# Kernel tuning notes

Measured on AMD Instinct MI355X. Metric: run time of the kernel, lower is better.

## Reference

```python
import jax, jax.numpy as jnp
import numpy as np

N_NODES = 50000
N_EDGES = 800000
D_S, D_R, D_E, D_X, D_P, NUM_CLASSES = 64, 16, 64, 16, 64, 10


def setup_inputs() -> dict:
    key = jax.random.key(0)
    ks = jax.random.split(key, 11)
    return {
        "O": jax.random.normal(ks[0], (N_NODES, D_S), dtype=jnp.float32),
        "X": jax.random.normal(ks[1], (N_NODES, D_X), dtype=jnp.float32),
        "R_a": jax.random.normal(ks[2], (N_EDGES, D_R), dtype=jnp.float32),
        "senders": jax.random.randint(ks[3], (N_EDGES,), 0, N_NODES, dtype=jnp.int32).astype(jnp.int64),
        "receivers": jax.random.randint(ks[4], (N_EDGES,), 0, N_NODES, dtype=jnp.int32).astype(jnp.int64),
        "W_r": jax.random.normal(ks[5], (2 * D_S + D_R, D_E), dtype=jnp.float32) * 0.05,
        "b_r": jax.random.normal(ks[6], (D_E,), dtype=jnp.float32) * 0.05,
        "W_o": jax.random.normal(ks[7], (D_S + D_X + D_E, D_P), dtype=jnp.float32) * 0.05,
        "b_o": jax.random.normal(ks[8], (D_P,), dtype=jnp.float32) * 0.05,
        "W_s": jax.random.normal(ks[9], (D_P, NUM_CLASSES), dtype=jnp.float32) * 0.05,
        "b_s": jax.random.normal(ks[10], (NUM_CLASSES,), dtype=jnp.float32) * 0.05,
    }


def reference(O, X, R_a, senders, receivers, W_r, b_r, W_o, b_o, W_s, b_s):
    n_nodes = O.shape[0]
    # marshalling: gather sender/receiver node states, concat relation attrs -> [E, 2*D_S + D_R]
    B = jnp.concatenate([O[senders], O[receivers], R_a], axis=-1)
    # relation model phi_r: per-edge effects [E, D_E]
    E = B @ W_r + b_r
    # scatter-aggregate edge effects onto receiver nodes -> [N, D_E]
    E_hat = jax.ops.segment_sum(E, receivers, num_segments=n_nodes)
    # object model phi_o on concat(state, external, aggregated effects)
    C = jnp.concatenate([O, X, E_hat], axis=-1)
    P = C @ W_o + b_o
    scores = P @ W_s + b_s
    probs = jax.nn.softmax(scores, axis=1)
    return probs
```

## Files before the change

kernel.cpp:

```cpp
#include <hip/hip_runtime.h>

#define N_NODES 50000
#define N_EDGES 800000

#define WS_A       ((size_t)0)
#define WS_COUNT   ((size_t)16384)
#define WS_CURSOR  ((size_t)216384)
#define WS_OFF     ((size_t)217088)
#define WS_RANK    ((size_t)417792)
#define WS_US      ((size_t)3618816)
#define WS_U01     ((size_t)6019072)
#define WS_WSORT   ((size_t)10019328)

__device__ __forceinline__ unsigned int f32_to_bf16_rne(float f) {
    unsigned int x = __float_as_uint(f);
    return (x + 0x7fffu + ((x >> 16) & 1u)) >> 16;
}

__global__ __launch_bounds__(256) void precompute_A(
    const float* __restrict__ W_r, const float* __restrict__ b_r,
    const float* __restrict__ W_o, const float* __restrict__ b_o,
    const float* __restrict__ W_s, const float* __restrict__ b_s,
    float* __restrict__ A)
{
    __shared__ float Wc2[640];
    const int t = threadIdx.x;

    for (int idx = t; idx < 640; idx += 256) {
        const int row = 80 + idx / 10, c = idx % 10;
        float acc = 0.f;
        for (int j = 0; j < 64; ++j)
            acc = fmaf(W_o[row * 64 + j], W_s[j * 10 + c], acc);
        Wc2[idx] = acc;
    }
    __syncthreads();

    for (int g = blockIdx.x * 256 + t; g < 3616; g += gridDim.x * 256) {
        if (g < 1356) {
            const int row = g / 6, c = 10 + g % 6;
            A[row * 16 + c] = 0.f;
        } else if (g < 2156) {
            const int i = g - 1356, row = i / 10, c = i % 10;
            float acc = 0.f;
            for (int j = 0; j < 64; ++j)
                acc = fmaf(W_o[row * 64 + j], W_s[j * 10 + c], acc);
            A[row * 16 + c] = acc;
        } else if (g < 3596) {
            const int i = g - 2156, k = i / 10, c = i % 10;
            const int wrow = (k < 64) ? k : (k < 80 ? 128 + (k - 64) : 64 + (k - 80));
            const int arow = (k < 64) ? 80 + k : (k < 80 ? 144 + (k - 64) : 160 + (k - 80));
            const float* src = W_r + (size_t)wrow * 64;
            float acc = 0.f;
            for (int m = 0; m < 64; ++m)
                acc = fmaf(src[m], Wc2[m * 10 + c], acc);
            A[arow * 16 + c] = acc;
        } else if (g < 3606) {
            const int c = g - 3596;
            float acc = 0.f;
            for (int m = 0; m < 64; ++m)
                acc = fmaf(b_r[m], Wc2[m * 10 + c], acc);
            A[224 * 16 + c] = acc;
        } else {
            const int c = g - 3606;
            float acc = b_s[c];
            for (int j = 0; j < 64; ++j)
                acc = fmaf(b_o[j], W_s[j * 10 + c], acc);
            A[225 * 16 + c] = acc;
        }
    }
}

__global__ __launch_bounds__(256) void node_u_kernel(
    const float* __restrict__ O, const float* __restrict__ X,
    const float* __restrict__ A,
    float* __restrict__ us, float* __restrict__ u01)
{
    __shared__ float2 lA[226 * 5];
    const int t = threadIdx.x;
    for (int i = t; i < 226 * 5; i += 256) {
        const int row = i / 5, cp = i - row * 5;
        lA[i] = *reinterpret_cast<const float2*>(A + (size_t)row * 16 + 2 * cp);
    }
    __syncthreads();

    const int tid = blockIdx.x * 256 + t;
    if (tid >= N_NODES * 5) return;
    const int n = tid / 5;
    const int cp = tid - n * 5;

    float vs0 = 0.f, vs1 = 0.f, v00 = 0.f, v01 = 0.f, v10 = 0.f, v11 = 0.f;

    const float4* Ov = reinterpret_cast<const float4*>(O + (size_t)n * 64);
#pragma unroll
    for (int kc = 0; kc < 16; ++kc) {
        const float4 o4 = Ov[kc];
#pragma unroll
        for (int j = 0; j < 4; ++j) {
            const float ov = (j == 0) ? o4.x : (j == 1) ? o4.y : (j == 2) ? o4.z : o4.w;
            const int k = kc * 4 + j;
            const float2 aO = lA[k * 5 + cp];
            const float2 aS = lA[(80 + k) * 5 + cp];
            const float2 aD = lA[(160 + k) * 5 + cp];
            v00 = fmaf(ov, aO.x, v00); v01 = fmaf(ov, aO.y, v01);
            vs0 = fmaf(ov, aS.x, vs0); vs1 = fmaf(ov, aS.y, vs1);
            v10 = fmaf(ov, aD.x, v10); v11 = fmaf(ov, aD.y, v11);
        }
    }
    const float4* Xv = reinterpret_cast<const float4*>(X + (size_t)n * 16);
#pragma unroll
    for (int kc = 0; kc < 4; ++kc) {
        const float4 x4 = Xv[kc];
#pragma unroll
        for (int j = 0; j < 4; ++j) {
            const float xv = (j == 0) ? x4.x : (j == 1) ? x4.y : (j == 2) ? x4.z : x4.w;
            const int k = 64 + kc * 4 + j;
            const float2 aX = lA[k * 5 + cp];
            v00 = fmaf(xv, aX.x, v00); v01 = fmaf(xv, aX.y, v01);
        }
    }

    const float2 c0 = lA[224 * 5 + cp];
    const float2 c1 = lA[225 * 5 + cp];
    *reinterpret_cast<float2*>(us + (size_t)n * 12 + 2 * cp) = make_float2(vs0, vs1);
    *reinterpret_cast<float2*>(u01 + (size_t)n * 20 + 2 * cp) =
        make_float2(v00 + c1.x, v01 + c1.y);
    *reinterpret_cast<float2*>(u01 + (size_t)n * 20 + 10 + 2 * cp) =
        make_float2(v10 + c0.x, v11 + c0.y);
}

__global__ __launch_bounds__(256) void count_rank_kernel(
    const int* __restrict__ receivers, int* __restrict__ count,
    int* __restrict__ rank)
{
    const int t = blockIdx.x * 256 + threadIdx.x;
    if (t * 4 >= N_EDGES) return;
    const int4 r4 = reinterpret_cast<const int4*>(receivers)[t];
    int4 k4;
    k4.x = atomicAdd(count + r4.x, 1);
    k4.y = atomicAdd(count + r4.y, 1);
    k4.z = atomicAdd(count + r4.z, 1);
    k4.w = atomicAdd(count + r4.w, 1);
    reinterpret_cast<int4*>(rank)[t] = k4;
}

__global__ __launch_bounds__(256) void alloc_kernel(
    const int* __restrict__ count, unsigned int* __restrict__ cursor,
    int* __restrict__ off)
{
    const int n = blockIdx.x * 256 + threadIdx.x;
    const int lane = threadIdx.x & 63;
    const int c = (n < N_NODES) ? count[n] : 0;

    int pre = c;
#pragma unroll
    for (int d = 1; d < 64; d <<= 1) {
        const int v = __shfl_up(pre, d);
        if (lane >= d) pre += v;
    }
    const int total = __shfl(pre, 63);
    int base = 0;
    if (lane == 63) base = (int)atomicAdd(cursor, (unsigned int)total);
    base = __shfl(base, 63);

    if (n < N_NODES) off[n] = base + pre - c;
}

__global__ __launch_bounds__(256) void edge_w_kernel(
    const float* __restrict__ R_a,
    const int* __restrict__ senders, const int* __restrict__ receivers,
    const int* __restrict__ rank, const int* __restrict__ off,
    const float* __restrict__ us, const float* __restrict__ A,
    unsigned int* __restrict__ wsort)
{
    const int e = blockIdx.x * blockDim.x + threadIdx.x;
    if (e >= N_EDGES) return;
    const int s = senders[e];
    const int r = receivers[e];
    const int pos = off[r] + rank[e];

    const float4* U = reinterpret_cast<const float4*>(us + (size_t)s * 12);
    const float4 ua = U[0];
    const float4 ub = U[1];
    const float4 uc = U[2];
    float a[10] = {ua.x, ua.y, ua.z, ua.w, ub.x, ub.y, ub.z, ub.w, uc.x, uc.y};

    const float4* Rv = reinterpret_cast<const float4*>(R_a + (size_t)e * 16);
#pragma unroll
    for (int kc = 0; kc < 4; ++kc) {
        const float4 b4 = Rv[kc];
        const float* A0 = A + (size_t)(144 + kc * 4) * 16;
#pragma unroll
        for (int c = 0; c < 10; ++c) a[c] = fmaf(b4.x, A0[c], a[c]);
#pragma unroll
        for (int c = 0; c < 10; ++c) a[c] = fmaf(b4.y, A0[16 + c], a[c]);
#pragma unroll
        for (int c = 0; c < 10; ++c) a[c] = fmaf(b4.z, A0[32 + c], a[c]);
#pragma unroll
        for (int c = 0; c < 10; ++c) a[c] = fmaf(b4.w, A0[48 + c], a[c]);
    }

    unsigned int* wp = wsort + (size_t)pos * 5;
    wp[0] = f32_to_bf16_rne(a[0]) | (f32_to_bf16_rne(a[1]) << 16);
    wp[1] = f32_to_bf16_rne(a[2]) | (f32_to_bf16_rne(a[3]) << 16);
    wp[2] = f32_to_bf16_rne(a[4]) | (f32_to_bf16_rne(a[5]) << 16);
    wp[3] = f32_to_bf16_rne(a[6]) | (f32_to_bf16_rne(a[7]) << 16);
    wp[4] = f32_to_bf16_rne(a[8]) | (f32_to_bf16_rne(a[9]) << 16);
}

__global__ __launch_bounds__(256) void node_score_kernel(
    const float* __restrict__ u01,
    const int* __restrict__ off, const int* __restrict__ count,
    const unsigned int* __restrict__ w,
    float* __restrict__ out)
{
    const int tid = blockIdx.x * 256 + threadIdx.x;
    const int n = tid >> 4;
    const int c = tid & 15;
    if (n >= N_NODES) return;

    const int cc = (c < 10) ? c : 0;
    const int half = cc >> 1;
    const int sh = (cc & 1) * 16;

    const int beg = off[n];
    const int dge = count[n];
    const int end = beg + dge;
    float sc = u01[(size_t)n * 20 + cc] + (float)dge * u01[(size_t)n * 20 + 10 + cc];

    float s0 = 0.f, s1 = 0.f, s2 = 0.f, s3 = 0.f;
    int i = beg;
    for (; i + 3 < end; i += 4) {
        const unsigned int v0 = w[(size_t)(i + 0) * 5 + half];
        const unsigned int v1 = w[(size_t)(i + 1) * 5 + half];
        const unsigned int v2 = w[(size_t)(i + 2) * 5 + half];
        const unsigned int v3 = w[(size_t)(i + 3) * 5 + half];
        s0 += __uint_as_float((v0 >> sh) << 16);
        s1 += __uint_as_float((v1 >> sh) << 16);
        s2 += __uint_as_float((v2 >> sh) << 16);
        s3 += __uint_as_float((v3 >> sh) << 16);
    }
    for (; i < end; ++i) {
        const unsigned int v = w[(size_t)i * 5 + half];
        s0 += __uint_as_float((v >> sh) << 16);
    }
    sc += (s0 + s1) + (s2 + s3);

    float m = (c < 10) ? sc : -3.0e38f;
#pragma unroll
    for (int d = 1; d < 16; d <<= 1) m = fmaxf(m, __shfl_xor(m, d, 16));
    const float ex = (c < 10) ? __expf(sc - m) : 0.f;
    float sum = ex;
#pragma unroll
    for (int d = 1; d < 16; d <<= 1) sum += __shfl_xor(sum, d, 16);
    if (c < 10) out[(size_t)n * 10 + c] = ex / sum;
}

extern "C" void kernel_launch(void* const* d_in, const int* in_sizes, int n_in,
                              void* d_out, int out_size, void* d_ws, size_t ws_size,
                              hipStream_t stream)
{
    const float* O    = (const float*)d_in[0];
    const float* X    = (const float*)d_in[1];
    const float* R_a  = (const float*)d_in[2];
    const int* senders   = (const int*)d_in[3];
    const int* receivers = (const int*)d_in[4];
    const float* W_r  = (const float*)d_in[5];
    const float* b_r  = (const float*)d_in[6];
    const float* W_o  = (const float*)d_in[7];
    const float* b_o  = (const float*)d_in[8];
    const float* W_s  = (const float*)d_in[9];
    const float* b_s  = (const float*)d_in[10];
    float* out = (float*)d_out;
    char* ws = (char*)d_ws;

    float* A      = (float*)(ws + WS_A);
    int* count    = (int*)(ws + WS_COUNT);
    unsigned int* cursor = (unsigned int*)(ws + WS_CURSOR);
    int* off      = (int*)(ws + WS_OFF);
    int* rank     = (int*)(ws + WS_RANK);
    float* us     = (float*)(ws + WS_US);
    float* u01    = (float*)(ws + WS_U01);
    unsigned int* wsort = (unsigned int*)(ws + WS_WSORT);

    hipMemsetAsync(count, 0, (size_t)(200000 + 4 + 384), stream);

    precompute_A<<<10, 256, 0, stream>>>(W_r, b_r, W_o, b_o, W_s, b_s, A);

    count_rank_kernel<<<(N_EDGES / 4 + 255) / 256, 256, 0, stream>>>(
        receivers, count, rank);

    alloc_kernel<<<(N_NODES + 255) / 256, 256, 0, stream>>>(count, cursor, off);

    node_u_kernel<<<(N_NODES * 5 + 255) / 256, 256, 0, stream>>>(O, X, A, us, u01);

    edge_w_kernel<<<(N_EDGES + 255) / 256, 256, 0, stream>>>(
        R_a, senders, receivers, rank, off, us, A, wsort);

    node_score_kernel<<<(N_NODES * 16 + 255) / 256, 256, 0, stream>>>(
        u01, off, count, wsort, out);
}
```

Before: 125.7 us.

## Replace per-node CSR sort with coarse 64-bin partition and LDS atomic reduction

Drops the per-receiver count/rank/offset pipeline, which needed global atomics on every edge plus a full node scan. Edges are now histogrammed into 64 bins of contiguous receivers, scattered per bin with block-local atomics, and each bin is reduced by a 1024-thread block using shared-memory float atomics before the softmax. This removes the node-level global atomics and the random CSR writes. In exchange, only 64 blocks run the final reduce, so GPU occupancy is low and LDS atomic contention rises. Float atomic accumulation order also becomes nondeterministic.

```diff
diff --git a/kernel.cpp b/kernel.cpp
--- a/kernel.cpp
+++ b/kernel.cpp
@@ -2,15 +2,18 @@
 
 #define N_NODES 50000
 #define N_EDGES 800000
+#define NBINS 64
+#define BIN_NODES 784
+#define EPB 1024
+#define NBLK_E ((N_EDGES + EPB - 1) / EPB)
 
 #define WS_A       ((size_t)0)
-#define WS_COUNT   ((size_t)16384)
-#define WS_CURSOR  ((size_t)216384)
-#define WS_OFF     ((size_t)217088)
-#define WS_RANK    ((size_t)417792)
-#define WS_US      ((size_t)3618816)
-#define WS_U01     ((size_t)6019072)
-#define WS_WSORT   ((size_t)10019328)
+#define WS_BCOUNT  ((size_t)16384)
+#define WS_BBASE   ((size_t)20480)
+#define WS_BCUR    ((size_t)20992)
+#define WS_US      ((size_t)65536)
+#define WS_U01     ((size_t)2465536)
+#define WS_PAY     ((size_t)6465536)
 
 __device__ __forceinline__ unsigned int f32_to_bf16_rne(float f) {
     unsigned int x = __float_as_uint(f);
@@ -128,131 +131,171 @@
         make_float2(v10 + c0.x, v11 + c0.y);
 }
 
-__global__ __launch_bounds__(256) void count_rank_kernel(
-    const int* __restrict__ receivers, int* __restrict__ count,
-    int* __restrict__ rank)
-{
-    const int t = blockIdx.x * 256 + threadIdx.x;
-    if (t * 4 >= N_EDGES) return;
-    const int4 r4 = reinterpret_cast<const int4*>(receivers)[t];
-    int4 k4;
-    k4.x = atomicAdd(count + r4.x, 1);
-    k4.y = atomicAdd(count + r4.y, 1);
-    k4.z = atomicAdd(count + r4.z, 1);
-    k4.w = atomicAdd(count + r4.w, 1);
-    reinterpret_cast<int4*>(rank)[t] = k4;
-}
-
-__global__ __launch_bounds__(256) void alloc_kernel(
-    const int* __restrict__ count, unsigned int* __restrict__ cursor,
-    int* __restrict__ off)
-{
-    const int n = blockIdx.x * 256 + threadIdx.x;
-    const int lane = threadIdx.x & 63;
-    const int c = (n < N_NODES) ? count[n] : 0;
-
-    int pre = c;
+__global__ __launch_bounds__(256) void hist_kernel(
+    const int* __restrict__ receivers, int* __restrict__ bcount)
+{
+    __shared__ int h[NBINS];
+    const int t = threadIdx.x;
+    if (t < NBINS) h[t] = 0;
+    __syncthreads();
+    const int t4 = blockIdx.x * 256 + t;
+    if (t4 * 4 < N_EDGES) {
+        const int4 r4 = reinterpret_cast<const int4*>(receivers)[t4];
+        atomicAdd(&h[r4.x / BIN_NODES], 1);
+        atomicAdd(&h[r4.y / BIN_NODES], 1);
+        atomicAdd(&h[r4.z / BIN_NODES], 1);
+        atomicAdd(&h[r4.w / BIN_NODES], 1);
+    }
+    __syncthreads();
+    if (t < NBINS && h[t] > 0) atomicAdd(bcount + t * 16, h[t]);
+}
+
+__global__ __launch_bounds__(64) void scan_kernel(
+    const int* __restrict__ bcount, int* __restrict__ bbase, int* __restrict__ bcur)
+{
+    const int t = threadIdx.x;
+    const int v = bcount[t * 16];
+    int pre = v;
 #pragma unroll
     for (int d = 1; d < 64; d <<= 1) {
-        const int v = __shfl_up(pre, d);
-        if (lane >= d) pre += v;
-    }
-    const int total = __shfl(pre, 63);
-    int base = 0;
-    if (lane == 63) base = (int)atomicAdd(cursor, (unsigned int)total);
-    base = __shfl(base, 63);
-
-    if (n < N_NODES) off[n] = base + pre - c;
-}
-
-__global__ __launch_bounds__(256) void edge_w_kernel(
+        const int u = __shfl_up(pre, d);
+        if (t >= d) pre += u;
+    }
+    const int ex = pre - v;
+    bbase[t] = ex;
+    bcur[t * 16] = ex;
+    if (t == 63) bbase[64] = pre;
+}
+
+__global__ __launch_bounds__(256) void bin_scatter_kernel(
     const float* __restrict__ R_a,
     const int* __restrict__ senders, const int* __restrict__ receivers,
-    const int* __restrict__ rank, const int* __restrict__ off,
     const float* __restrict__ us, const float* __restrict__ A,
-    unsigned int* __restrict__ wsort)
-{
-    const int e = blockIdx.x * blockDim.x + threadIdx.x;
-    if (e >= N_EDGES) return;
-    const int s = senders[e];
-    const int r = receivers[e];
-    const int pos = off[r] + rank[e];
-
-    const float4* U = reinterpret_cast<const float4*>(us + (size_t)s * 12);
-    const float4 ua = U[0];
-    const float4 ub = U[1];
-    const float4 uc = U[2];
-    float a[10] = {ua.x, ua.y, ua.z, ua.w, ub.x, ub.y, ub.z, ub.w, uc.x, uc.y};
-
-    const float4* Rv = reinterpret_cast<const float4*>(R_a + (size_t)e * 16);
-#pragma unroll
-    for (int kc = 0; kc < 4; ++kc) {
-        const float4 b4 = Rv[kc];
-        const float* A0 = A + (size_t)(144 + kc * 4) * 16;
-#pragma unroll
-        for (int c = 0; c < 10; ++c) a[c] = fmaf(b4.x, A0[c], a[c]);
-#pragma unroll
-        for (int c = 0; c < 10; ++c) a[c] = fmaf(b4.y, A0[16 + c], a[c]);
-#pragma unroll
-        for (int c = 0; c < 10; ++c) a[c] = fmaf(b4.z, A0[32 + c], a[c]);
-#pragma unroll
-        for (int c = 0; c < 10; ++c) a[c] = fmaf(b4.w, A0[48 + c], a[c]);
-    }
-
-    unsigned int* wp = wsort + (size_t)pos * 5;
-    wp[0] = f32_to_bf16_rne(a[0]) | (f32_to_bf16_rne(a[1]) << 16);
-    wp[1] = f32_to_bf16_rne(a[2]) | (f32_to_bf16_rne(a[3]) << 16);
-    wp[2] = f32_to_bf16_rne(a[4]) | (f32_to_bf16_rne(a[5]) << 16);
-    wp[3] = f32_to_bf16_rne(a[6]) | (f32_to_bf16_rne(a[7]) << 16);
-    wp[4] = f32_to_bf16_rne(a[8]) | (f32_to_bf16_rne(a[9]) << 16);
-}
-
-__global__ __launch_bounds__(256) void node_score_kernel(
+    int* __restrict__ bcur,
+    unsigned int* __restrict__ pay)
+{
+    __shared__ int h[NBINS];
+    __shared__ int basep[NBINS];
+    __shared__ int cur[NBINS];
+    const int t = threadIdx.x;
+    if (t < NBINS) h[t] = 0;
+    __syncthreads();
+
+    const int e0 = blockIdx.x * EPB + t * 4;
+    const bool valid = (e0 < N_EDGES);
+    int4 r4 = make_int4(0, 0, 0, 0);
+    int b0 = 0, b1 = 0, b2 = 0, b3 = 0;
+    if (valid) {
+        r4 = reinterpret_cast<const int4*>(receivers)[e0 >> 2];
+        b0 = r4.x / BIN_NODES; b1 = r4.y / BIN_NODES;
+        b2 = r4.z / BIN_NODES; b3 = r4.w / BIN_NODES;
+        atomicAdd(&h[b0], 1); atomicAdd(&h[b1], 1);
+        atomicAdd(&h[b2], 1); atomicAdd(&h[b3], 1);
+    }
+    __syncthreads();
+    if (t < NBINS) {
+        const int c = h[t];
+        basep[t] = (c > 0) ? atomicAdd(bcur + t * 16, c) : 0;
+        cur[t] = 0;
+    }
+    __syncthreads();
+    if (!valid) return;
+
+    const int4 s4 = reinterpret_cast<const int4*>(senders)[e0 >> 2];
+
+#pragma unroll
+    for (int j = 0; j < 4; ++j) {
+        const int e = e0 + j;
+        const int r = (j == 0) ? r4.x : (j == 1) ? r4.y : (j == 2) ? r4.z : r4.w;
+        const int s = (j == 0) ? s4.x : (j == 1) ? s4.y : (j == 2) ? s4.z : s4.w;
+        const int b = (j == 0) ? b0 : (j == 1) ? b1 : (j == 2) ? b2 : b3;
+        const int nl = r - b * BIN_NODES;
+        const int rk = atomicAdd(&cur[b], 1);
+        const int pos = basep[b] + rk;
+
+        const float4* U = reinterpret_cast<const float4*>(us + (size_t)s * 12);
+        const float4 ua = U[0], ub = U[1], uc = U[2];
+        float a[10] = {ua.x, ua.y, ua.z, ua.w, ub.x, ub.y, ub.z, ub.w, uc.x, uc.y};
+
+        const float4* Rv = reinterpret_cast<const float4*>(R_a + (size_t)e * 16);
+#pragma unroll
+        for (int kc = 0; kc < 4; ++kc) {
+            const float4 b4 = Rv[kc];
+            const float* A0 = A + (size_t)(144 + kc * 4) * 16;
+#pragma unroll
+            for (int c = 0; c < 10; ++c) a[c] = fmaf(b4.x, A0[c], a[c]);
+#pragma unroll
+            for (int c = 0; c < 10; ++c) a[c] = fmaf(b4.y, A0[16 + c], a[c]);
+#pragma unroll
+            for (int c = 0; c < 10; ++c) a[c] = fmaf(b4.z, A0[32 + c], a[c]);
+#pragma unroll
+            for (int c = 0; c < 10; ++c) a[c] = fmaf(b4.w, A0[48 + c], a[c]);
+        }
+
+        unsigned int* wp = pay + (size_t)pos * 6;
+        uint2 q0, q1, q2;
+        q0.x = f32_to_bf16_rne(a[0]) | (f32_to_bf16_rne(a[1]) << 16);
+        q0.y = f32_to_bf16_rne(a[2]) | (f32_to_bf16_rne(a[3]) << 16);
+        q1.x = f32_to_bf16_rne(a[4]) | (f32_to_bf16_rne(a[5]) << 16);
+        q1.y = f32_to_bf16_rne(a[6]) | (f32_to_bf16_rne(a[7]) << 16);
+        q2.x = f32_to_bf16_rne(a[8]) | (f32_to_bf16_rne(a[9]) << 16);
+        q2.y = (unsigned int)nl;
+        reinterpret_cast<uint2*>(wp)[0] = q0;
+        reinterpret_cast<uint2*>(wp)[1] = q1;
+        reinterpret_cast<uint2*>(wp)[2] = q2;
+    }
+}
+
+__global__ __launch_bounds__(1024) void bin_reduce_kernel(
+    const unsigned int* __restrict__ pay,
+    const int* __restrict__ bbase,
     const float* __restrict__ u01,
-    const int* __restrict__ off, const int* __restrict__ count,
-    const unsigned int* __restrict__ w,
     float* __restrict__ out)
 {
-    const int tid = blockIdx.x * 256 + threadIdx.x;
-    const int n = tid >> 4;
-    const int c = tid & 15;
-    if (n >= N_NODES) return;
-
-    const int cc = (c < 10) ? c : 0;
-    const int half = cc >> 1;
-    const int sh = (cc & 1) * 16;
-
-    const int beg = off[n];
-    const int dge = count[n];
-    const int end = beg + dge;
-    float sc = u01[(size_t)n * 20 + cc] + (float)dge * u01[(size_t)n * 20 + 10 + cc];
-
-    float s0 = 0.f, s1 = 0.f, s2 = 0.f, s3 = 0.f;
-    int i = beg;
-    for (; i + 3 < end; i += 4) {
-        const unsigned int v0 = w[(size_t)(i + 0) * 5 + half];
-        const unsigned int v1 = w[(size_t)(i + 1) * 5 + half];
-        const unsigned int v2 = w[(size_t)(i + 2) * 5 + half];
-        const unsigned int v3 = w[(size_t)(i + 3) * 5 + half];
-        s0 += __uint_as_float((v0 >> sh) << 16);
-        s1 += __uint_as_float((v1 >> sh) << 16);
-        s2 += __uint_as_float((v2 >> sh) << 16);
-        s3 += __uint_as_float((v3 >> sh) << 16);
-    }
-    for (; i < end; ++i) {
-        const unsigned int v = w[(size_t)i * 5 + half];
-        s0 += __uint_as_float((v >> sh) << 16);
-    }
-    sc += (s0 + s1) + (s2 + s3);
-
-    float m = (c < 10) ? sc : -3.0e38f;
-#pragma unroll
-    for (int d = 1; d < 16; d <<= 1) m = fmaxf(m, __shfl_xor(m, d, 16));
-    const float ex = (c < 10) ? __expf(sc - m) : 0.f;
-    float sum = ex;
-#pragma unroll
-    for (int d = 1; d < 16; d <<= 1) sum += __shfl_xor(sum, d, 16);
-    if (c < 10) out[(size_t)n * 10 + c] = ex / sum;
+    __shared__ float acc[BIN_NODES * 10];
+    __shared__ int   deg[BIN_NODES];
+    const int b = blockIdx.x;
+    const int t = threadIdx.x;
+
+    for (int i = t; i < BIN_NODES * 10; i += 1024) acc[i] = 0.f;
+    for (int i = t; i < BIN_NODES; i += 1024) deg[i] = 0;
+    __syncthreads();
+
+    const int lo = bbase[b];
+    const int cnt = bbase[b + 1] - lo;
+    const int gid = t >> 4, lane = t & 15;
+
+    for (int i = gid; i < cnt; i += 64) {
+        const unsigned int* rec = pay + (size_t)(lo + i) * 6;
+        const unsigned int nl = rec[5];
+        if (lane < 10) {
+            const unsigned int dw = rec[lane >> 1];
+            const float w = __uint_as_float((dw >> ((lane & 1) * 16)) << 16);
+            atomicAdd(&acc[nl * 10 + lane], w);
+        } else if (lane == 10) {
+            atomicAdd(&deg[nl], 1);
+        }
+    }
+    __syncthreads();
+
+    for (int nl = gid; nl < BIN_NODES; nl += 64) {
+        const int n = b * BIN_NODES + nl;
+        if (n < N_NODES) {
+            const int cc = (lane < 10) ? lane : 0;
+            const float dg = (float)deg[nl];
+            float sc = u01[(size_t)n * 20 + cc]
+                     + dg * u01[(size_t)n * 20 + 10 + cc]
+                     + acc[nl * 10 + cc];
+            float m = (lane < 10) ? sc : -3.0e38f;
+#pragma unroll
+            for (int d = 1; d < 16; d <<= 1) m = fmaxf(m, __shfl_xor(m, d, 16));
+            const float ex = (lane < 10) ? __expf(sc - m) : 0.f;
+            float sum = ex;
+#pragma unroll
+            for (int d = 1; d < 16; d <<= 1) sum += __shfl_xor(sum, d, 16);
+            if (lane < 10) out[(size_t)n * 10 + lane] = ex / sum;
+        }
+    }
 }
 
 extern "C" void kernel_launch(void* const* d_in, const int* in_sizes, int n_in,
@@ -274,28 +317,25 @@
     char* ws = (char*)d_ws;
 
     float* A      = (float*)(ws + WS_A);
-    int* count    = (int*)(ws + WS_COUNT);
-    unsigned int* cursor = (unsigned int*)(ws + WS_CURSOR);
-    int* off      = (int*)(ws + WS_OFF);
-    int* rank     = (int*)(ws + WS_RANK);
+    int* bcount   = (int*)(ws + WS_BCOUNT);
+    int* bbase    = (int*)(ws + WS_BBASE);
+    int* bcur     = (int*)(ws + WS_BCUR);
     float* us     = (float*)(ws + WS_US);
     float* u01    = (float*)(ws + WS_U01);
-    unsigned int* wsort = (unsigned int*)(ws + WS_WSORT);
-
-    hipMemsetAsync(count, 0, (size_t)(200000 + 4 + 384), stream);
+    unsigned int* pay = (unsigned int*)(ws + WS_PAY);
+
+    hipMemsetAsync(bcount, 0, (size_t)4096, stream);
 
     precompute_A<<<10, 256, 0, stream>>>(W_r, b_r, W_o, b_o, W_s, b_s, A);
 
-    count_rank_kernel<<<(N_EDGES / 4 + 255) / 256, 256, 0, stream>>>(
-        receivers, count, rank);
-
-    alloc_kernel<<<(N_NODES + 255) / 256, 256, 0, stream>>>(count, cursor, off);
-
     node_u_kernel<<<(N_NODES * 5 + 255) / 256, 256, 0, stream>>>(O, X, A, us, u01);
 
-    edge_w_kernel<<<(N_EDGES + 255) / 256, 256, 0, stream>>>(
-        R_a, senders, receivers, rank, off, us, A, wsort);
-
-    node_score_kernel<<<(N_NODES * 16 + 255) / 256, 256, 0, stream>>>(
-        u01, off, count, wsort, out);
-}
+    hist_kernel<<<NBLK_E, 256, 0, stream>>>(receivers, bcount);
+
+    scan_kernel<<<1, 64, 0, stream>>>(bcount, bbase, bcur);
+
+    bin_scatter_kernel<<<NBLK_E, 256, 0, stream>>>(
+        R_a, senders, receivers, us, A, bcur, pay);
+
+    bin_reduce_kernel<<<NBINS, 1024, 0, stream>>>(pay, bbase, u01, out);
+}
```

After: 298.9 us. +137.7%, slower.
